# Kernel optimization log

Hardware: AMD Instinct MI355X
Metric: run time of the kernel (lower is better)

## Reference

```python
import jax, jax.numpy as jnp
import numpy as np

HEADS = 8
DIM_HEAD = 64
SCALE = DIM_HEAD ** -0.5
POS_DIM = 64


def _sincos_pe(H, W, dim, dtype):
    # matches build_2d_sincos_pos_embed: [1, dim, H, W]
    y = jnp.linspace(-1.0, 1.0, H)[:, None] * jnp.ones((1, W), jnp.float32)
    x = jnp.ones((H, 1), jnp.float32) * jnp.linspace(-1.0, 1.0, W)[None, :]
    omega = 1.0 / (10000.0 ** (jnp.arange(dim // 4, dtype=jnp.float32) / (dim // 4)))
    px = x[..., None] * omega  # [H, W, dim//4]
    py = y[..., None] * omega
    pe = jnp.concatenate([jnp.sin(px), jnp.cos(px), jnp.sin(py), jnp.cos(py)], axis=-1)
    return pe.transpose(2, 0, 1)[None].astype(dtype)


def _conv2d(x, w):
    return jax.lax.conv_general_dilated(
        x, w, (1, 1), 'SAME', dimension_numbers=('NCHW', 'OIHW', 'NCHW'))


def _sobel(d):
    kx = jnp.array([[1, 0, -1], [2, 0, -2], [1, 0, -1]], jnp.float32).reshape(1, 1, 3, 3)
    ky = jnp.array([[1, 2, 1], [0, 0, 0], [-1, -2, -1]], jnp.float32).reshape(1, 1, 3, 3)
    return _conv2d(d, kx), _conv2d(d, ky)


def setup_inputs() -> dict:
    key = jax.random.key(0)
    ks = jax.random.split(key, 8)
    B, C, H, W = 2, 256, 64, 64
    hid = HEADS * DIM_HEAD  # 512
    s = 0.02
    return {
        'x': jax.random.normal(ks[0], (B, C, H, W), jnp.float32),
        'dsm': jax.random.uniform(ks[1], (B, 1, H, W), jnp.float32),
        'wq': jax.random.normal(ks[2], (hid, C), jnp.float32) * s,
        'wkv': jax.random.normal(ks[3], (2 * hid, C + 1), jnp.float32) * s,
        'wout': jax.random.normal(ks[4], (C, hid), jnp.float32) * s,
        'bout': jnp.zeros((C,), jnp.float32),
        'w_hape': jax.random.normal(ks[5], (hid, POS_DIM + 3), jnp.float32) * s,
        'b_hape': jnp.zeros((hid,), jnp.float32),
        'w_alpha': jax.random.normal(ks[6], (1, 1, 3, 3), jnp.float32) * 0.1,
        'b_alpha': jnp.zeros((1,), jnp.float32),
    }


def reference(x, dsm, wq, wkv, wout, bout, w_hape, b_hape, w_alpha, b_alpha):
    B, C, H, W = x.shape
    hid = wq.shape[0]
    # per-sample min-max normalize DSM over spatial dims
    dmin = dsm.min(axis=(2, 3), keepdims=True)
    dmax = dsm.max(axis=(2, 3), keepdims=True)
    d = (dsm - dmin) / (dmax - dmin + 1e-6)
    # HAPE: [PE | h | grad_h] -> 1x1 conv to hidden
    pe = jnp.broadcast_to(_sincos_pe(H, W, POS_DIM, x.dtype), (B, POS_DIM, H, W))
    gx, gy = _sobel(d)
    hape_in = jnp.concatenate([pe, d, gx, gy], axis=1)  # [B, 67, H, W]
    hape_k = jnp.einsum('oc,bchw->bohw', w_hape, hape_in) + b_hape[None, :, None, None]
    # QKV via 1x1 convs
    q = jnp.einsum('oc,bchw->bohw', wq, x)
    kv = jnp.einsum('oc,bchw->bohw', wkv, jnp.concatenate([x, d], axis=1))
    k = kv[:, :hid] + hape_k
    v = kv[:, hid:]
    to_heads = lambda t: t.reshape(B, HEADS, DIM_HEAD, H * W)  # b (h c) x y -> b h c (xy)
    qh = to_heads(q) * SCALE
    kh = to_heads(k)
    vh = to_heads(v)
    sim = jnp.einsum('bhdi,bhdj->bhij', qh, kh)  # [B, h, N, N]
    attn = jax.nn.softmax(sim, axis=-1)
    out = jnp.einsum('bhij,bhdj->bhid', attn, vh)  # [B, h, N, d]
    # b h (x y) d -> b (h d) x y
    out = out.transpose(0, 1, 3, 2).reshape(B, HEADS * DIM_HEAD, H, W)
    out = jnp.einsum('oc,bchw->bohw', wout, out) + bout[None, :, None, None]
    # fine: gradient-magnitude alpha gating
    mag = jnp.sqrt(jnp.maximum(gx, 0.0) ** 2 + jnp.maximum(gy, 0.0) ** 2 + 1e-12)
    alpha = jax.nn.sigmoid(_conv2d(mag, w_alpha) + b_alpha[None, :, None, None])
    return x + out * alpha
```

## Files before the change

kernel.cpp:

```cpp
#include <hip/hip_runtime.h>
#include <math.h>

#define NPOS 4096
#define MTOT 8192
#define KP   352
#define HT 64
#define WT 64
#define NSPLIT 2
#define KEYS_PER (NPOS / NSPLIT)
#define NCH (KEYS_PER / 64)

typedef unsigned short ushortT;
typedef short v8s __attribute__((ext_vector_type(8)));
typedef float v4f __attribute__((ext_vector_type(4)));
typedef unsigned uint2v __attribute__((ext_vector_type(2)));

static __device__ __forceinline__ ushortT bfr(float f) {
    union { float f; unsigned u; } v; v.f = f;
    return (ushortT)((v.u + 0x8000u) >> 16);
}
static __device__ __forceinline__ unsigned pack2bf(float a, float b) {
    union { float f; unsigned u; } ua, ub; ua.f = a; ub.f = b;
    return __builtin_amdgcn_perm(ub.u + 0x8000u, ua.u + 0x8000u, 0x07060302u);
}
static __device__ __forceinline__ unsigned pack2bf_t(float a, float b) {
    union { float f; unsigned u; } ua, ub; ua.f = a; ub.f = b;
    return __builtin_amdgcn_perm(ub.u, ua.u, 0x07060302u);
}
static __device__ __forceinline__ float fexp2(float x) {
#if __has_builtin(__builtin_amdgcn_exp2f)
    return __builtin_amdgcn_exp2f(x);
#else
    return exp2f(x);
#endif
}

__global__ void k_prep(const float* __restrict__ dsm,
                       const float* __restrict__ walpha, const float* __restrict__ balpha,
                       ushortT* __restrict__ F, float* __restrict__ alpha) {
    __shared__ ushortT tab[64][32];
    __shared__ float smn[4], smx[4];

    int idx = blockIdx.x * 256 + threadIdx.x;
    int b = idx / NPOS, n = idx % NPOS;
    int hh = n / WT, ww = n % WT;
    const float* dp = dsm + (size_t)b * NPOS;
    const float l2w = 13.287712379549449f;

    {
        int t = threadIdx.x;
        #pragma unroll
        for (int e8 = 0; e8 < 8; e8++) {
            int e = t * 8 + e8;
            int c = e >> 5, j = e & 31, i = j & 15;
            float coord = -1.f + 2.f * (float)c / 63.f;
            float omega = exp2f(-(float)i * (l2w / 16.f));
            float v = (j < 16) ? __sinf(coord * omega) : __cosf(coord * omega);
            tab[c][j] = bfr(v);
        }
    }

    float mn = 1e30f, mx = -1e30f;
    for (int i = threadIdx.x; i < NPOS; i += 256) {
        float v = dp[i];
        mn = fminf(mn, v); mx = fmaxf(mx, v);
    }
    for (int off = 32; off; off >>= 1) {
        mn = fminf(mn, __shfl_xor(mn, off, 64));
        mx = fmaxf(mx, __shfl_xor(mx, off, 64));
    }
    int wid = threadIdx.x >> 6;
    if ((threadIdx.x & 63) == 0) { smn[wid] = mn; smx[wid] = mx; }
    __syncthreads();
    float dmin = fminf(fminf(smn[0], smn[1]), fminf(smn[2], smn[3]));
    float dmax = fmaxf(fmaxf(smx[0], smx[1]), fmaxf(smx[2], smx[3]));
    float inv = 1.0f / (dmax - dmin + 1e-6f);

    float dwin[5][5];
    #pragma unroll
    for (int dy = 0; dy < 5; dy++)
        #pragma unroll
        for (int dx = 0; dx < 5; dx++) {
            int y = hh + dy - 2, x = ww + dx - 2;
            float v = 0.0f;
            if (y >= 0 && y < HT && x >= 0 && x < WT) v = (dp[y * WT + x] - dmin) * inv;
            dwin[dy][dx] = v;
        }

    float gxc = 0.f, gyc = 0.f;
    float conv = 0.f;
    #pragma unroll
    for (int oy = 0; oy < 3; oy++)
        #pragma unroll
        for (int ox = 0; ox < 3; ox++) {
            int qy = hh + oy - 1, qx = ww + ox - 1;
            float m = 0.0f;
            if (qy >= 0 && qy < HT && qx >= 0 && qx < WT) {
                float gx = dwin[oy][ox] - dwin[oy][ox + 2]
                         + 2.f * dwin[oy + 1][ox] - 2.f * dwin[oy + 1][ox + 2]
                         + dwin[oy + 2][ox] - dwin[oy + 2][ox + 2];
                float gy = dwin[oy][ox] + 2.f * dwin[oy][ox + 1] + dwin[oy][ox + 2]
                         - dwin[oy + 2][ox] - 2.f * dwin[oy + 2][ox + 1] - dwin[oy + 2][ox + 2];
                if (oy == 1 && ox == 1) { gxc = gx; gyc = gy; }
                float rx = fmaxf(gx, 0.f), ry = fmaxf(gy, 0.f);
                m = sqrtf(rx * rx + ry * ry + 1e-12f);
            }
            conv += walpha[oy * 3 + ox] * m;
        }
    alpha[idx] = 1.f / (1.f + __expf(-(conv + balpha[0])));

    ushortT* fb = F + (size_t)idx * KP;
    fb[256] = bfr(dwin[2][2]);
    fb[257] = bfr(gxc);
    fb[258] = bfr(gyc);
    #pragma unroll
    for (int i = 0; i < 32; i++) fb[259 + i] = tab[ww][i];
    #pragma unroll
    for (int i = 0; i < 32; i++) fb[291 + i] = tab[hh][i];
    #pragma unroll
    for (int z = 323; z < KP; z++) fb[z] = 0;
}

__global__ void k_cast(const float* __restrict__ x, ushortT* __restrict__ F) {
    __shared__ __align__(16) ushortT Tl[64][72];
    int nt = blockIdx.x * 64;
    int b = blockIdx.y >> 2, ct = (blockIdx.y & 3) * 64;
    int t = threadIdx.x;
    #pragma unroll
    for (int rep = 0; rep < 4; rep++) {
        int row = rep * 16 + (t >> 4), c4 = (t & 15) * 4;
        float4 f4 = *(const float4*)&x[((size_t)(b * 256 + ct + row)) * NPOS + nt + c4];
        Tl[c4 + 0][row] = bfr(f4.x);
        Tl[c4 + 1][row] = bfr(f4.y);
        Tl[c4 + 2][row] = bfr(f4.z);
        Tl[c4 + 3][row] = bfr(f4.w);
    }
    __syncthreads();
    #pragma unroll
    for (int rep = 0; rep < 2; rep++) {
        int slot = rep * 256 + t, row = slot >> 3, c8 = slot & 7;
        *(uint4*)&F[((size_t)(b * 4096 + nt + row)) * KP + ct + c8 * 8] = *(uint4*)&Tl[row][c8 * 8];
    }
}

__global__ void k_wcprep(const float* __restrict__ wq, const float* __restrict__ wkv,
                         const float* __restrict__ whape, const float* __restrict__ bhape,
                         const float* __restrict__ wout,
                         ushortT* __restrict__ Wc, float* __restrict__ biasc,
                         ushortT* __restrict__ woutb) {
    int idx = blockIdx.x * 256 + threadIdx.x;
    if (blockIdx.x < 512) {
        woutb[idx] = bfr(wout[idx]);
    }
    int o = idx / KP, k = idx % KP;
    float v = 0.f;
    if (o < 512) {
        if (k < 256) v = wq[o * 256 + k] * 0.18033688011112042f;
        if (k == 0) biasc[o] = 0.f;
    } else if (o < 1024) {
        int r = o - 512;
        if (k < 257) v = wkv[r * 257 + k];
        if (k == 256)      v += whape[r * 67 + 64];
        else if (k == 257) v = whape[r * 67 + 65];
        else if (k == 258) v = whape[r * 67 + 66];
        else if (k >= 259 && k < 323) v = whape[r * 67 + (k - 259)];
        if (k == 0) biasc[o] = bhape[r];
    } else {
        int r = o - 512;
        if (k < 257) v = wkv[r * 257 + k];
        if (k == 0) biasc[o] = 0.f;
    }
    Wc[idx] = bfr(v);
}

__global__ __launch_bounds__(256) void k_gemm1(const ushortT* __restrict__ Wc, const ushortT* __restrict__ F,
                                               const float* __restrict__ biasc,
                                               ushortT* __restrict__ qT, ushortT* __restrict__ kT,
                                               ushortT* __restrict__ vv) {
    __shared__ __align__(16) ushortT Al[128][40];
    __shared__ __align__(16) ushortT Bl[64][40];
    __shared__ __align__(16) ushortT Vt[128][72];
    int mt = blockIdx.x * 64;
    int ot = blockIdx.y * 128;
    int t = threadIdx.x, w = t >> 6, lane = t & 63, u = lane & 15, quad = lane >> 4;
    int ar0 = t >> 2, ac0 = t & 3;
    int ar1 = 64 + ar0;
    int br = t >> 2, bc = t & 3;
    v4f acc[2][4] = {};
    for (int k0 = 0; k0 < KP; k0 += 32) {
        __syncthreads();
        *(uint4*)&Al[ar0][ac0 * 8] = *(const uint4*)&Wc[(size_t)(ot + ar0) * KP + k0 + ac0 * 8];
        *(uint4*)&Al[ar1][ac0 * 8] = *(const uint4*)&Wc[(size_t)(ot + ar1) * KP + k0 + ac0 * 8];
        *(uint4*)&Bl[br][bc * 8]   = *(const uint4*)&F[(size_t)(mt + br) * KP + k0 + bc * 8];
        __syncthreads();
        v8s a0 = *(v8s*)&Al[w * 32 + u][quad * 8];
        v8s a1 = *(v8s*)&Al[w * 32 + 16 + u][quad * 8];
        #pragma unroll
        for (int n4 = 0; n4 < 4; n4++) {
            v8s bb = *(v8s*)&Bl[n4 * 16 + u][quad * 8];
            acc[0][n4] = __builtin_amdgcn_mfma_f32_16x16x32_bf16(a0, bb, acc[0][n4], 0, 0, 0);
            acc[1][n4] = __builtin_amdgcn_mfma_f32_16x16x32_bf16(a1, bb, acc[1][n4], 0, 0, 0);
        }
    }
    float bo[2][4];
    #pragma unroll
    for (int rr = 0; rr < 2; rr++)
        #pragma unroll
        for (int r = 0; r < 4; r++) bo[rr][r] = biasc[ot + w * 32 + rr * 16 + quad * 4 + r];
    if (ot < 1024) {
        ushortT* dst = (ot < 512) ? qT : kT;
        #pragma unroll
        for (int rr = 0; rr < 2; rr++) {
            int oo = ot + w * 32 + rr * 16;
            int h = (oo >> 6) & 7;
            int dcol = (oo & 63) + quad * 4;
            #pragma unroll
            for (int n4 = 0; n4 < 4; n4++) {
                int m = mt + n4 * 16 + u;
                uint2 val;
                val.x = pack2bf(acc[rr][n4][0] + bo[rr][0], acc[rr][n4][1] + bo[rr][1]);
                val.y = pack2bf(acc[rr][n4][2] + bo[rr][2], acc[rr][n4][3] + bo[rr][3]);
                *(uint2*)&dst[((size_t)h * MTOT + m) * 64 + dcol] = val;
            }
        }
    } else {
        __syncthreads();
        #pragma unroll
        for (int rr = 0; rr < 2; rr++)
            #pragma unroll
            for (int n4 = 0; n4 < 4; n4++) {
                int ml = n4 * 16 + u;
                #pragma unroll
                for (int r = 0; r < 4; r++)
                    Vt[w * 32 + rr * 16 + quad * 4 + r][ml] = bfr(acc[rr][n4][r] + bo[rr][r]);
            }
        __syncthreads();
        #pragma unroll
        for (int rep = 0; rep < 4; rep++) {
            int slot = rep * 256 + t, row = slot >> 3, c8 = slot & 7;
            *(uint4*)&vv[(size_t)(ot - 1024 + row) * MTOT + mt + c8 * 8] = *(uint4*)&Vt[row][c8 * 8];
        }
    }
}

#define LIDX(row, cb) (((row) << 6) + ((((cb) ^ ((row) & 7))) << 3))
__global__ __launch_bounds__(256, 4) void k_flash(const ushortT* __restrict__ qT,
                                                  const ushortT* __restrict__ kT,
                                                  const ushortT* __restrict__ vv,
                                                  float* __restrict__ Opart,
                                                  float* __restrict__ liPart) {
    __shared__ __align__(16) ushortT Kbuf[2][64 * 64];
    __shared__ __align__(16) ushortT Vbuf[2][64 * 64];

    int it = blockIdx.x;
    int bh = blockIdx.y;
    int half = blockIdx.z;
    int b = bh >> 3, h = bh & 7;
    int colbase = b * NPOS;
    int t = threadIdx.x, w = t >> 6, lane = t & 63, u = lane & 15, quad = lane >> 4;
    int qb = it * 128 + w * 32;

    const ushortT* Qg = qT + ((size_t)h * MTOT + colbase + qb) * 64;
    const ushortT* Kg = kT + ((size_t)h * MTOT + colbase + half * KEYS_PER) * 64;
    const ushortT* Vg = vv + ((size_t)(h * 64)) * MTOT + colbase + half * KEYS_PER;

    int row0 = t >> 3, c80 = t & 7;
    int row1 = 32 + row0;

    unsigned boff[4][2];
    #pragma unroll
    for (int i4 = 0; i4 < 4; i4++) {
        boff[i4][0] = 2u * (unsigned)LIDX(i4 * 16 + u, quad);
        boff[i4][1] = 2u * (unsigned)LIDX(i4 * 16 + u, 4 + quad);
        asm volatile("" : "+v"(boff[i4][0]), "+v"(boff[i4][1]));
    }
    unsigned woff0 = 2u * (unsigned)LIDX(row0, c80);
    unsigned woff1 = 2u * (unsigned)LIDX(row1, c80);
    asm volatile("" : "+v"(woff0), "+v"(woff1));

    v8s bq[2][2];
    #pragma unroll
    for (int g = 0; g < 2; g++)
        #pragma unroll
        for (int hf = 0; hf < 2; hf++)
            bq[g][hf] = *(const v8s*)&Qg[(size_t)(g * 16 + u) * 64 + hf * 32 + quad * 8];

    v8s ones;
    #pragma unroll
    for (int i = 0; i < 8; i++) ones[i] = (short)0x3F80;

    v4f li4[2] = {};
    v4f O[4][2] = {};

    uint4 kr0 = *(const uint4*)&Kg[(size_t)row0 * 64 + c80 * 8];
    uint4 kr1 = *(const uint4*)&Kg[(size_t)row1 * 64 + c80 * 8];
    uint4 vr0 = *(const uint4*)&Vg[(size_t)row0 * MTOT + c80 * 8];
    uint4 vr1 = *(const uint4*)&Vg[(size_t)row1 * MTOT + c80 * 8];

    #pragma unroll 2
    for (int jc = 0; jc < NCH; jc++) {
        int cur = jc & 1;
        char* KbW = (char*)&Kbuf[cur][0];
        char* VbW = (char*)&Vbuf[cur][0];
        *(uint4*)(KbW + woff0) = kr0;
        *(uint4*)(KbW + woff1) = kr1;
        *(uint4*)(VbW + woff0) = vr0;
        *(uint4*)(VbW + woff1) = vr1;
        __syncthreads();
        if (jc + 1 < NCH) {
            int jb = (jc + 1) * 64;
            kr0 = *(const uint4*)&Kg[(size_t)(jb + row0) * 64 + c80 * 8];
            kr1 = *(const uint4*)&Kg[(size_t)(jb + row1) * 64 + c80 * 8];
            vr0 = *(const uint4*)&Vg[(size_t)row0 * MTOT + jb + c80 * 8];
            vr1 = *(const uint4*)&Vg[(size_t)row1 * MTOT + jb + c80 * 8];
        }

        const char* Kb = (const char*)&Kbuf[cur][0];
        const char* Vb = (const char*)&Vbuf[cur][0];

        v8s bp[2][2];
        #pragma unroll
        for (int kp = 0; kp < 2; kp++) {
            unsigned pk0[2][2], pk1[2][2];
            #pragma unroll
            for (int kk = 0; kk < 2; kk++) {
                int k4 = kp * 2 + kk;
                v8s ak0 = *(const v8s*)(Kb + boff[k4][0]);
                v8s ak1 = *(const v8s*)(Kb + boff[k4][1]);
                v4f st[2];
                __builtin_amdgcn_s_setprio(1);
                #pragma unroll
                for (int g = 0; g < 2; g++) {
                    st[g] = (v4f){0.f, 0.f, 0.f, 0.f};
                    st[g] = __builtin_amdgcn_mfma_f32_16x16x32_bf16(ak0, bq[g][0], st[g], 0, 0, 0);
                    st[g] = __builtin_amdgcn_mfma_f32_16x16x32_bf16(ak1, bq[g][1], st[g], 0, 0, 0);
                }
                __builtin_amdgcn_s_setprio(0);
                #pragma unroll
                for (int g = 0; g < 2; g++) {
                    float p0 = fexp2(st[g][0]);
                    float p1 = fexp2(st[g][1]);
                    float p2 = fexp2(st[g][2]);
                    float p3 = fexp2(st[g][3]);
                    pk0[g][kk] = pack2bf_t(p0, p1);
                    pk1[g][kk] = pack2bf_t(p2, p3);
                }
            }
            #pragma unroll
            for (int g = 0; g < 2; g++) {
                uint2v r0s = __builtin_amdgcn_permlane32_swap(pk0[g][0], pk0[g][1], false, false);
                uint2v r1s = __builtin_amdgcn_permlane32_swap(pk1[g][0], pk1[g][1], false, false);
                uint2v t0 = __builtin_amdgcn_permlane16_swap(r0s.x, r0s.y, false, false);
                uint2v t1 = __builtin_amdgcn_permlane16_swap(r1s.x, r1s.y, false, false);
                union { uint4 u4; v8s s; } cv;
                cv.u4.x = t0.x; cv.u4.y = t1.x; cv.u4.z = t0.y; cv.u4.w = t1.y;
                bp[g][kp] = cv.s;
            }
        }

        __builtin_amdgcn_s_setprio(1);
        #pragma unroll
        for (int g = 0; g < 2; g++) {
            li4[g] = __builtin_amdgcn_mfma_f32_16x16x32_bf16(ones, bp[g][0], li4[g], 0, 0, 0);
            li4[g] = __builtin_amdgcn_mfma_f32_16x16x32_bf16(ones, bp[g][1], li4[g], 0, 0, 0);
        }
        #pragma unroll
        for (int d4 = 0; d4 < 4; d4++) {
            v8s av0 = *(const v8s*)(Vb + boff[d4][0]);
            v8s av1 = *(const v8s*)(Vb + boff[d4][1]);
            #pragma unroll
            for (int g = 0; g < 2; g++) {
                O[d4][g] = __builtin_amdgcn_mfma_f32_16x16x32_bf16(av0, bp[g][0], O[d4][g], 0, 0, 0);
                O[d4][g] = __builtin_amdgcn_mfma_f32_16x16x32_bf16(av1, bp[g][1], O[d4][g], 0, 0, 0);
            }
        }
        __builtin_amdgcn_s_setprio(0);
    }

    #pragma unroll
    for (int g = 0; g < 2; g++) {
        int q = qb + g * 16 + u;
        size_t m2 = (size_t)(half * 2 + b) * 4096 + q;
        size_t base = m2 * 512 + h * 64;
        #pragma unroll
        for (int d4 = 0; d4 < 4; d4++) {
            float4 o4;
            o4.x = O[d4][g][0]; o4.y = O[d4][g][1]; o4.z = O[d4][g][2]; o4.w = O[d4][g][3];
            *(float4*)&Opart[base + d4 * 16 + quad * 4] = o4;
        }
        if (quad == 0) liPart[m2 * 8 + h] = li4[g][0];
    }
}

__global__ __launch_bounds__(256) void k_comb(const float* __restrict__ Opart,
                                              const float* __restrict__ liPart,
                                              ushortT* __restrict__ aoB) {
    int tid = blockIdx.x * 256 + threadIdx.x;
    int m = tid >> 7, c4 = (tid & 127) * 4, h = c4 >> 6;
    float l = 0.f;
    #pragma unroll
    for (int s = 0; s < NSPLIT; s++) l += liPart[((size_t)s * 8192 + m) * 8 + h];
    float inv = 1.f / l;
    float ox = 0.f, oy = 0.f, oz = 0.f, ow = 0.f;
    #pragma unroll
    for (int s = 0; s < NSPLIT; s++) {
        float4 o = *(const float4*)&Opart[((size_t)s * 8192 + m) * 512 + c4];
        ox += o.x; oy += o.y; oz += o.z; ow += o.w;
    }
    uint2 val;
    val.x = pack2bf(ox * inv, oy * inv);
    val.y = pack2bf(oz * inv, ow * inv);
    *(uint2*)&aoB[(size_t)m * 512 + c4] = val;
}

__global__ __launch_bounds__(256) void k_gemm2(const ushortT* __restrict__ woutb, const ushortT* __restrict__ aoB,
                                               const float* __restrict__ bout, const float* __restrict__ x,
                                               const float* __restrict__ alpha, float* __restrict__ out) {
    __shared__ __align__(16) ushortT Al[64][40];
    __shared__ __align__(16) ushortT Bl[64][40];
    int mt = blockIdx.x * 64;
    int ot = blockIdx.y * 64;
    int t = threadIdx.x, w = t >> 6, lane = t & 63, u = lane & 15, quad = lane >> 4;
    int arow = t >> 2, ac8 = t & 3;
    v4f acc[4] = {};
    for (int k0 = 0; k0 < 512; k0 += 32) {
        __syncthreads();
        *(uint4*)&Al[arow][ac8 * 8] = *(const uint4*)&woutb[(size_t)(ot + arow) * 512 + k0 + ac8 * 8];
        *(uint4*)&Bl[arow][ac8 * 8] = *(const uint4*)&aoB[(size_t)(mt + arow) * 512 + k0 + ac8 * 8];
        __syncthreads();
        v8s a = *(v8s*)&Al[w * 16 + u][quad * 8];
        #pragma unroll
        for (int n4 = 0; n4 < 4; n4++) {
            v8s bb = *(v8s*)&Bl[n4 * 16 + u][quad * 8];
            acc[n4] = __builtin_amdgcn_mfma_f32_16x16x32_bf16(a, bb, acc[n4], 0, 0, 0);
        }
    }
    int b = mt >> 12, n0 = mt & 4095;
    int obase = ot + w * 16 + quad * 4;
    float bo[4];
    #pragma unroll
    for (int r = 0; r < 4; r++) bo[r] = bout[obase + r];
    #pragma unroll
    for (int n4 = 0; n4 < 4; n4++) {
        int n = n0 + n4 * 16 + u;
        float al = alpha[(size_t)b * NPOS + n];
        #pragma unroll
        for (int r = 0; r < 4; r++) {
            size_t xi = ((size_t)(b * 256 + obase + r)) * NPOS + n;
            out[xi] = x[xi] + (acc[n4][r] + bo[r]) * al;
        }
    }
}

extern "C" void kernel_launch(void* const* d_in, const int* in_sizes, int n_in,
                              void* d_out, int out_size, void* d_ws, size_t ws_size,
                              hipStream_t stream) {
    const float* x      = (const float*)d_in[0];
    const float* dsm    = (const float*)d_in[1];
    const float* wq     = (const float*)d_in[2];
    const float* wkv    = (const float*)d_in[3];
    const float* wout   = (const float*)d_in[4];
    const float* bout   = (const float*)d_in[5];
    const float* whape  = (const float*)d_in[6];
    const float* bhape  = (const float*)d_in[7];
    const float* walpha = (const float*)d_in[8];
    const float* balpha = (const float*)d_in[9];
    float* out = (float*)d_out;
    float* ws  = (float*)d_ws;

    size_t off = 0;
    float* alpha = ws + off; off += (size_t)2 * NPOS;
    float* biasc = ws + off; off += 2048;
    float* Opart  = ws + off; off += (size_t)NSPLIT * MTOT * 512;
    float* liPart = ws + off; off += (size_t)NSPLIT * MTOT * 8;
    ushortT* F     = (ushortT*)(ws + off); off += (size_t)MTOT * KP / 2;
    ushortT* Wc    = (ushortT*)(ws + off); off += (size_t)1536 * KP / 2;
    ushortT* woutb = (ushortT*)(ws + off); off += (size_t)256 * 512 / 2;
    ushortT* qT    = (ushortT*)(ws + off); off += (size_t)8 * MTOT * 64 / 2;
    ushortT* kT    = (ushortT*)(ws + off); off += (size_t)8 * MTOT * 64 / 2;
    ushortT* vv    = (ushortT*)(ws + off); off += (size_t)512 * MTOT / 2;
    ushortT* aoB   = (ushortT*)(ws + off); off += (size_t)MTOT * 512 / 2;
    (void)in_sizes; (void)n_in; (void)out_size; (void)ws_size;

    k_prep<<<32, 256, 0, stream>>>(dsm, walpha, balpha, F, alpha);
    k_cast<<<dim3(64, 8), 256, 0, stream>>>(x, F);
    k_wcprep<<<(1536 * KP) / 256, 256, 0, stream>>>(wq, wkv, whape, bhape, wout, Wc, biasc, woutb);
    k_gemm1<<<dim3(128, 12), 256, 0, stream>>>(Wc, F, biasc, qT, kT, vv);
    k_flash<<<dim3(32, 16, NSPLIT), 256, 0, stream>>>(qT, kT, vv, Opart, liPart);
    k_comb<<<4096, 256, 0, stream>>>(Opart, liPart, aoB);
    k_gemm2<<<dim3(128, 4), 256, 0, stream>>>(woutb, aoB, bout, x, alpha, out);
}
```

Before: 205.2 us.

## Widen gemm1 output tile to 256 rows and store flash partials in bf16

k_gemm1 now computes 256 output channels per block instead of 128, giving a 4x4 MFMA accumulator grid per wave for more A/B reuse and half as many blocks. Shared memory is aliased between the staging tiles and the V transpose buffer. Separately, the flash-attention partial outputs are written as bf16 instead of fp32, and k_comb unpacks them, halving the traffic of the split-K combine. This trades precision of the unnormalised partial sums, and the larger gemm1 tile raises register pressure and lowers the block count to 768.

```diff
diff --git a/kernel.cpp b/kernel.cpp
--- a/kernel.cpp
+++ b/kernel.cpp
@@ -33,6 +33,12 @@
 #else
     return exp2f(x);
 #endif
+}
+static __device__ __forceinline__ float bflo(unsigned u) {
+    union { unsigned u; float f; } v; v.u = u << 16; return v.f;
+}
+static __device__ __forceinline__ float bfhi(unsigned u) {
+    union { unsigned u; float f; } v; v.u = u & 0xffff0000u; return v.f;
 }
 
 __global__ void k_prep(const float* __restrict__ dsm,
@@ -177,41 +183,48 @@
                                                const float* __restrict__ biasc,
                                                ushortT* __restrict__ qT, ushortT* __restrict__ kT,
                                                ushortT* __restrict__ vv) {
-    __shared__ __align__(16) ushortT Al[128][40];
-    __shared__ __align__(16) ushortT Bl[64][40];
-    __shared__ __align__(16) ushortT Vt[128][72];
+    __shared__ __align__(16) char smem[256 * 72 * 2];
+    ushortT (*Al)[40] = (ushortT(*)[40])smem;
+    ushortT (*Bl)[40] = (ushortT(*)[40])(smem + 20480);
+    ushortT (*Vt)[72] = (ushortT(*)[72])smem;
+
     int mt = blockIdx.x * 64;
-    int ot = blockIdx.y * 128;
+    int ot = blockIdx.y * 256;
     int t = threadIdx.x, w = t >> 6, lane = t & 63, u = lane & 15, quad = lane >> 4;
-    int ar0 = t >> 2, ac0 = t & 3;
-    int ar1 = 64 + ar0;
-    int br = t >> 2, bc = t & 3;
-    v4f acc[2][4] = {};
+    v4f acc[4][4] = {};
     for (int k0 = 0; k0 < KP; k0 += 32) {
         __syncthreads();
-        *(uint4*)&Al[ar0][ac0 * 8] = *(const uint4*)&Wc[(size_t)(ot + ar0) * KP + k0 + ac0 * 8];
-        *(uint4*)&Al[ar1][ac0 * 8] = *(const uint4*)&Wc[(size_t)(ot + ar1) * KP + k0 + ac0 * 8];
-        *(uint4*)&Bl[br][bc * 8]   = *(const uint4*)&F[(size_t)(mt + br) * KP + k0 + bc * 8];
-        __syncthreads();
-        v8s a0 = *(v8s*)&Al[w * 32 + u][quad * 8];
-        v8s a1 = *(v8s*)&Al[w * 32 + 16 + u][quad * 8];
-        #pragma unroll
-        for (int n4 = 0; n4 < 4; n4++) {
-            v8s bb = *(v8s*)&Bl[n4 * 16 + u][quad * 8];
-            acc[0][n4] = __builtin_amdgcn_mfma_f32_16x16x32_bf16(a0, bb, acc[0][n4], 0, 0, 0);
-            acc[1][n4] = __builtin_amdgcn_mfma_f32_16x16x32_bf16(a1, bb, acc[1][n4], 0, 0, 0);
-        }
-    }
-    float bo[2][4];
-    #pragma unroll
-    for (int rr = 0; rr < 2; rr++)
-        #pragma unroll
-        for (int r = 0; r < 4; r++) bo[rr][r] = biasc[ot + w * 32 + rr * 16 + quad * 4 + r];
+        #pragma unroll
+        for (int rep = 0; rep < 4; rep++) {
+            int s = rep * 256 + t, row = s >> 2, ch = s & 3;
+            *(uint4*)&Al[row][ch * 8] = *(const uint4*)&Wc[(size_t)(ot + row) * KP + k0 + ch * 8];
+        }
+        {
+            int row = t >> 2, ch = t & 3;
+            *(uint4*)&Bl[row][ch * 8] = *(const uint4*)&F[(size_t)(mt + row) * KP + k0 + ch * 8];
+        }
+        __syncthreads();
+        v8s a[4], bb[4];
+        #pragma unroll
+        for (int rr = 0; rr < 4; rr++) a[rr] = *(v8s*)&Al[w * 64 + rr * 16 + u][quad * 8];
+        #pragma unroll
+        for (int n4 = 0; n4 < 4; n4++) bb[n4] = *(v8s*)&Bl[n4 * 16 + u][quad * 8];
+        #pragma unroll
+        for (int rr = 0; rr < 4; rr++)
+            #pragma unroll
+            for (int n4 = 0; n4 < 4; n4++)
+                acc[rr][n4] = __builtin_amdgcn_mfma_f32_16x16x32_bf16(a[rr], bb[n4], acc[rr][n4], 0, 0, 0);
+    }
+    float bo[4][4];
+    #pragma unroll
+    for (int rr = 0; rr < 4; rr++)
+        #pragma unroll
+        for (int r = 0; r < 4; r++) bo[rr][r] = biasc[ot + w * 64 + rr * 16 + quad * 4 + r];
     if (ot < 1024) {
         ushortT* dst = (ot < 512) ? qT : kT;
         #pragma unroll
-        for (int rr = 0; rr < 2; rr++) {
-            int oo = ot + w * 32 + rr * 16;
+        for (int rr = 0; rr < 4; rr++) {
+            int oo = ot + w * 64 + rr * 16;
             int h = (oo >> 6) & 7;
             int dcol = (oo & 63) + quad * 4;
             #pragma unroll
@@ -226,17 +239,17 @@
     } else {
         __syncthreads();
         #pragma unroll
-        for (int rr = 0; rr < 2; rr++)
+        for (int rr = 0; rr < 4; rr++)
             #pragma unroll
             for (int n4 = 0; n4 < 4; n4++) {
                 int ml = n4 * 16 + u;
                 #pragma unroll
                 for (int r = 0; r < 4; r++)
-                    Vt[w * 32 + rr * 16 + quad * 4 + r][ml] = bfr(acc[rr][n4][r] + bo[rr][r]);
+                    Vt[w * 64 + rr * 16 + quad * 4 + r][ml] = bfr(acc[rr][n4][r] + bo[rr][r]);
             }
         __syncthreads();
         #pragma unroll
-        for (int rep = 0; rep < 4; rep++) {
+        for (int rep = 0; rep < 8; rep++) {
             int slot = rep * 256 + t, row = slot >> 3, c8 = slot & 7;
             *(uint4*)&vv[(size_t)(ot - 1024 + row) * MTOT + mt + c8 * 8] = *(uint4*)&Vt[row][c8 * 8];
         }
@@ -247,7 +260,7 @@
 __global__ __launch_bounds__(256, 4) void k_flash(const ushortT* __restrict__ qT,
                                                   const ushortT* __restrict__ kT,
                                                   const ushortT* __restrict__ vv,
-                                                  float* __restrict__ Opart,
+                                                  ushortT* __restrict__ Opart,
                                                   float* __restrict__ liPart) {
     __shared__ __align__(16) ushortT Kbuf[2][64 * 64];
     __shared__ __align__(16) ushortT Vbuf[2][64 * 64];
@@ -384,15 +397,16 @@
         size_t base = m2 * 512 + h * 64;
         #pragma unroll
         for (int d4 = 0; d4 < 4; d4++) {
-            float4 o4;
-            o4.x = O[d4][g][0]; o4.y = O[d4][g][1]; o4.z = O[d4][g][2]; o4.w = O[d4][g][3];
-            *(float4*)&Opart[base + d4 * 16 + quad * 4] = o4;
+            uint2 o2;
+            o2.x = pack2bf(O[d4][g][0], O[d4][g][1]);
+            o2.y = pack2bf(O[d4][g][2], O[d4][g][3]);
+            *(uint2*)&Opart[base + d4 * 16 + quad * 4] = o2;
         }
         if (quad == 0) liPart[m2 * 8 + h] = li4[g][0];
     }
 }
 
-__global__ __launch_bounds__(256) void k_comb(const float* __restrict__ Opart,
+__global__ __launch_bounds__(256) void k_comb(const ushortT* __restrict__ Opart,
                                               const float* __restrict__ liPart,
                                               ushortT* __restrict__ aoB) {
     int tid = blockIdx.x * 256 + threadIdx.x;
@@ -404,8 +418,9 @@
     float ox = 0.f, oy = 0.f, oz = 0.f, ow = 0.f;
     #pragma unroll
     for (int s = 0; s < NSPLIT; s++) {
-        float4 o = *(const float4*)&Opart[((size_t)s * 8192 + m) * 512 + c4];
-        ox += o.x; oy += o.y; oz += o.z; ow += o.w;
+        uint2 o = *(const uint2*)&Opart[((size_t)s * 8192 + m) * 512 + c4];
+        ox += bflo(o.x); oy += bfhi(o.x);
+        oz += bflo(o.y); ow += bfhi(o.y);
     }
     uint2 val;
     val.x = pack2bf(ox * inv, oy * inv);
@@ -471,8 +486,8 @@
     size_t off = 0;
     float* alpha = ws + off; off += (size_t)2 * NPOS;
     float* biasc = ws + off; off += 2048;
-    float* Opart  = ws + off; off += (size_t)NSPLIT * MTOT * 512;
     float* liPart = ws + off; off += (size_t)NSPLIT * MTOT * 8;
+    ushortT* Opart = (ushortT*)(ws + off); off += (size_t)NSPLIT * MTOT * 512 / 2;
     ushortT* F     = (ushortT*)(ws + off); off += (size_t)MTOT * KP / 2;
     ushortT* Wc    = (ushortT*)(ws + off); off += (size_t)1536 * KP / 2;
     ushortT* woutb = (ushortT*)(ws + off); off += (size_t)256 * 512 / 2;
@@ -485,7 +500,7 @@
     k_prep<<<32, 256, 0, stream>>>(dsm, walpha, balpha, F, alpha);
     k_cast<<<dim3(64, 8), 256, 0, stream>>>(x, F);
     k_wcprep<<<(1536 * KP) / 256, 256, 0, stream>>>(wq, wkv, whape, bhape, wout, Wc, biasc, woutb);
-    k_gemm1<<<dim3(128, 12), 256, 0, stream>>>(Wc, F, biasc, qT, kT, vv);
+    k_gemm1<<<dim3(128, 6), 256, 0, stream>>>(Wc, F, biasc, qT, kT, vv);
     k_flash<<<dim3(32, 16, NSPLIT), 256, 0, stream>>>(qT, kT, vv, Opart, liPart);
     k_comb<<<4096, 256, 0, stream>>>(Opart, liPart, aoB);
     k_gemm2<<<dim3(128, 4), 256, 0, stream>>>(woutb, aoB, bout, x, alpha, out);
```

After: 206.8 us. About the same (+0.8%).
